# Kernel tuning notes

Measured on AMD Instinct MI355X. Metric: run time of the kernel, lower is better.

The kernel has to match this reference:

```python
import jax, jax.numpy as jnp
import numpy as np

B, T, D = 4, 2048, 1024
EPS = 1e-5


def _layernorm(x, g, b):
    mu = jnp.mean(x, axis=-1, keepdims=True)
    var = jnp.var(x, axis=-1, keepdims=True)
    return (x - mu) * jax.lax.rsqrt(var + EPS) * g + b


def setup_inputs() -> dict:
    key = jax.random.key(0)
    ks = jax.random.split(key, 16)
    s = lambda fan_in: 1.0 / np.sqrt(fan_in)
    return {
        "x": jax.random.normal(ks[0], (B, T, D), dtype=jnp.float32),
        "ln1_g": jnp.ones((D,), jnp.float32),
        "ln1_b": jnp.zeros((D,), jnp.float32),
        "Wqkv": jax.random.uniform(ks[1], (D, 3 * D), jnp.float32, -s(D), s(D)),
        "bqkv": jnp.zeros((3 * D,), jnp.float32),
        "Wproj": jax.random.uniform(ks[2], (D, D), jnp.float32, -s(D), s(D)),
        "bproj": jnp.zeros((D,), jnp.float32),
        "ln2_g": jnp.ones((D,), jnp.float32),
        "ln2_b": jnp.zeros((D,), jnp.float32),
        "W1": jax.random.uniform(ks[3], (D, 4 * D), jnp.float32, -s(D), s(D)),
        "b1": jnp.zeros((4 * D,), jnp.float32),
        "W2": jax.random.uniform(ks[4], (4 * D, D), jnp.float32, -s(4 * D), s(4 * D)),
        "b2": jnp.zeros((D,), jnp.float32),
    }


def reference(x, ln1_g, ln1_b, Wqkv, bqkv, Wproj, bproj, ln2_g, ln2_b, W1, b1, W2, b2):
    # NOTE: no residual connections in the original Block.
    h = _layernorm(x, ln1_g, ln1_b)
    kqv = h @ Wqkv + bqkv                      # [B,T,3D]
    k, q, v = jnp.split(kqv, 3, axis=-1)       # split order: k, q, v
    # Original scales by 1/sqrt(k.size(-1)) AFTER transposing k -> 1/sqrt(T).
    scores = jnp.einsum("btd,bsd->bts", q, k) * (1.0 / np.sqrt(T))
    causal = jnp.tril(jnp.ones((T, T), dtype=bool))
    scores = jnp.where(causal, scores, -jnp.inf)
    attn = jax.nn.softmax(scores, axis=-1)
    a = jnp.einsum("bts,bsd->btd", attn, v)
    a = a @ Wproj + bproj
    h2 = _layernorm(a, ln2_g, ln2_b)
    m = jax.nn.gelu(h2 @ W1 + b1, approximate=True)
    return m @ W2 + b2
```

## Files before the change

kernel.cpp:

```cpp
#include <hip/hip_runtime.h>
#include <hip/hip_bf16.h>

typedef __hip_bfloat16 bf16;
typedef __bf16 bf16x8 __attribute__((ext_vector_type(8)));
typedef __bf16 bf16x4 __attribute__((ext_vector_type(4)));
typedef float f32x4 __attribute__((ext_vector_type(4)));

static constexpr int Bq = 4, Tq = 2048, Dq = 1024;

__device__ inline float b2f(bf16 h) { return __bfloat162float(h); }
__device__ inline bf16 f2b(float f) { return __float2bfloat16(f); }

__device__ __forceinline__ void gload_lds16(const bf16* g, bf16* lds_wave_base) {
    __builtin_amdgcn_global_load_lds((const __attribute__((address_space(1))) void*)g,
                                     (__attribute__((address_space(3))) void*)lds_wave_base,
                                     16, 0, 0);
}

__device__ __forceinline__ float fast_gelu(float x) {
    float u = x * (0.7978845608028654f + 0.03567740814183427f * x * x);
    float e = __builtin_amdgcn_exp2f(-2.885390081777927f * u);
    return x * __builtin_amdgcn_rcpf(1.f + e);
}

__device__ inline void ld4f(const float* p, float* v) {
    float4 t = *reinterpret_cast<const float4*>(p);
    v[0] = t.x; v[1] = t.y; v[2] = t.z; v[3] = t.w;
}
__device__ inline void ld4f(const bf16* p, float* v) {
    bf16x4 t = *reinterpret_cast<const bf16x4*>(p);
    v[0] = (float)t[0]; v[1] = (float)t[1]; v[2] = (float)t[2]; v[3] = (float)t[3];
}

template <typename Tin>
__global__ void ln_kernel(const Tin* __restrict__ x, const float* __restrict__ g,
                          const float* __restrict__ b, bf16* __restrict__ out)
{
    const int row = blockIdx.x;
    const int tid = threadIdx.x;
    const int s0 = tid * 4;
    const Tin* xr = x + (size_t)row * Dq;
    bf16* orow = out + (size_t)row * Dq;
    float v[4], gv[4], bv[4];
    ld4f(xr + s0, v);
    ld4f(g + s0, gv);
    ld4f(b + s0, bv);
    float sum = v[0] + v[1] + v[2] + v[3];
    float sq = v[0]*v[0] + v[1]*v[1] + v[2]*v[2] + v[3]*v[3];
    for (int o = 32; o > 0; o >>= 1) { sum += __shfl_xor(sum, o); sq += __shfl_xor(sq, o); }
    __shared__ float ssum[4], ssq[4];
    const int w = tid >> 6;
    if ((tid & 63) == 0) { ssum[w] = sum; ssq[w] = sq; }
    __syncthreads();
    const float ts = ssum[0] + ssum[1] + ssum[2] + ssum[3];
    const float tq = ssq[0] + ssq[1] + ssq[2] + ssq[3];
    const float mean = ts / Dq;
    const float rs = rsqrtf(tq / Dq - mean * mean + 1e-5f);
    bf16x4 o4;
    #pragma unroll
    for (int i = 0; i < 4; ++i) o4[i] = (__bf16)((v[i] - mean) * rs * gv[i] + bv[i]);
    *reinterpret_cast<bf16x4*>(orow + s0) = o4;
}

__global__ void transpose_f2b_kernel(const float* __restrict__ in, bf16* __restrict__ out,
                                     long ldin, long ldout)
{
    __shared__ float tile[32][33];
    const int c0 = blockIdx.x * 32, r0 = blockIdx.y * 32;
    const int tx = threadIdx.x, ty = threadIdx.y;
    for (int i = 0; i < 4; ++i) {
        int r = r0 + ty + i * 8;
        tile[ty + i * 8][tx] = in[(size_t)r * ldin + c0 + tx];
    }
    __syncthreads();
    for (int i = 0; i < 4; ++i) {
        int cc = ty + i * 8;
        out[(size_t)(c0 + cc) * ldout + r0 + tx] = f2b(tile[tx][cc]);
    }
}

__global__ void transpose_b2b_kernel(const bf16* __restrict__ in, bf16* __restrict__ out,
                                     long ldin, long ldout, long inBatch, long outBatch)
{
    __shared__ bf16 tile[32][33];
    const bf16* ip = in + (size_t)blockIdx.z * inBatch;
    bf16* op = out + (size_t)blockIdx.z * outBatch;
    const int c0 = blockIdx.x * 32, r0 = blockIdx.y * 32;
    const int tx = threadIdx.x, ty = threadIdx.y;
    for (int i = 0; i < 4; ++i) {
        int r = r0 + ty + i * 8;
        tile[ty + i * 8][tx] = ip[(size_t)r * ldin + c0 + tx];
    }
    __syncthreads();
    for (int i = 0; i < 4; ++i) {
        int cc = ty + i * 8;
        op[(size_t)(c0 + cc) * ldout + r0 + tx] = tile[tx][cc];
    }
}

__global__ void softmax_kernel(bf16* __restrict__ attn)
{
    const int row = blockIdx.x;
    const int bb = row >> 11;
    const int t = row & (Tq - 1);
    bf16* base = attn + (size_t)bb * Tq * Tq + (size_t)t * Tq;
    const int tid = threadIdx.x;
    const int len = t + 1;
    const int s0 = tid * 8;
    bf16x8 v8 = *reinterpret_cast<const bf16x8*>(base + s0);
    float ev[8];
    #pragma unroll
    for (int i = 0; i < 8; ++i) ev[i] = (s0 + i < len) ? (float)v8[i] : -1e30f;
    float mx = ev[0];
    #pragma unroll
    for (int i = 1; i < 8; ++i) mx = fmaxf(mx, ev[i]);
    for (int o = 32; o > 0; o >>= 1) mx = fmaxf(mx, __shfl_xor(mx, o));
    __shared__ float sred[4];
    const int w = tid >> 6;
    if ((tid & 63) == 0) sred[w] = mx;
    __syncthreads();
    mx = fmaxf(fmaxf(sred[0], sred[1]), fmaxf(sred[2], sred[3]));
    __syncthreads();
    float sum = 0.f;
    #pragma unroll
    for (int i = 0; i < 8; ++i) {
        ev[i] = (s0 + i < len) ? __builtin_amdgcn_exp2f(1.4426950408889634f * (ev[i] - mx)) : 0.f;
        sum += ev[i];
    }
    for (int o = 32; o > 0; o >>= 1) sum += __shfl_xor(sum, o);
    if ((tid & 63) == 0) sred[w] = sum;
    __syncthreads();
    const float inv = __builtin_amdgcn_rcpf(sred[0] + sred[1] + sred[2] + sred[3]);
    bf16x8 o8;
    #pragma unroll
    for (int i = 0; i < 8; ++i) o8[i] = (__bf16)(ev[i] * inv);
    *reinterpret_cast<bf16x8*>(base + s0) = o8;
}

__global__ void gemm128(const bf16* __restrict__ A, const bf16* __restrict__ Bt,
                        const float* __restrict__ bias,
                        bf16* __restrict__ Cb, float* __restrict__ Cf,
                        int K, long lda, long ldb, long ldc,
                        long sA, long sB, long sC,
                        float scale, int act, int causal, int causalK)
{
    const int gx = gridDim.x, gy = gridDim.y;
    int lin = blockIdx.x + gx * blockIdx.y;
    const int band = lin & 7;
    const int idx = lin >> 3;
    const int bx = idx % gx;
    const int by = band * (gy >> 3) + idx / gx;

    const int m0 = by * 128, n0 = bx * 128;
    if (causal && n0 > m0 + 127) return;
    const int Kend = causalK ? min(K, m0 + 128) : K;

    __shared__ bf16 As[128 * 32];
    __shared__ bf16 Bs[128 * 32];

    const bf16* Ab = A + (size_t)blockIdx.z * sA;
    const bf16* Bb = Bt + (size_t)blockIdx.z * sB;
    const int tid = threadIdx.x;
    const int wid = tid >> 6, lane = tid & 63;
    const int wr = wid >> 1, wc = wid & 1;
    const int l15 = lane & 15, quad = lane >> 4;

    const int srow = wid * 16 + (lane >> 2);
    const int scol = (((lane & 3) ^ ((srow >> 1) & 3))) * 8;
    const bf16* agp0 = Ab + (size_t)(m0 + srow) * lda + scol;
    const bf16* agp1 = Ab + (size_t)(m0 + 64 + srow) * lda + scol;
    const bf16* bgp0 = Bb + (size_t)(n0 + srow) * ldb + scol;
    const bf16* bgp1 = Bb + (size_t)(n0 + 64 + srow) * ldb + scol;
    bf16* aw0 = As + wid * 512;
    bf16* aw1 = As + 2048 + wid * 512;
    bf16* bw0 = Bs + wid * 512;
    bf16* bw1 = Bs + 2048 + wid * 512;

    const int xsw = (l15 >> 1) & 3;
    const int afo = (wr * 64 + l15) * 32 + (quad ^ xsw) * 8;
    const int bfo = (wc * 64 + l15) * 32 + (quad ^ xsw) * 8;

    f32x4 acc[4][4];
    #pragma unroll
    for (int i = 0; i < 4; ++i)
        #pragma unroll
        for (int j = 0; j < 4; ++j) acc[i][j] = (f32x4){0.f, 0.f, 0.f, 0.f};

    for (int k0 = 0; k0 < Kend; k0 += 32) {
        gload_lds16(agp0 + k0, aw0);
        gload_lds16(agp1 + k0, aw1);
        gload_lds16(bgp0 + k0, bw0);
        gload_lds16(bgp1 + k0, bw1);
        __syncthreads();

        bf16x8 af[4], bff[4];
        #pragma unroll
        for (int i = 0; i < 4; ++i) af[i] = *reinterpret_cast<const bf16x8*>(As + afo + i * 512);
        #pragma unroll
        for (int j = 0; j < 4; ++j) bff[j] = *reinterpret_cast<const bf16x8*>(Bs + bfo + j * 512);
        #pragma unroll
        for (int i = 0; i < 4; ++i)
            #pragma unroll
            for (int j = 0; j < 4; ++j)
                acc[i][j] = __builtin_amdgcn_mfma_f32_16x16x32_bf16(af[i], bff[j], acc[i][j], 0, 0, 0);

        __syncthreads();
    }

    #pragma unroll
    for (int i = 0; i < 4; ++i) {
        const int row = m0 + wr * 64 + i * 16 + quad * 4;
        #pragma unroll
        for (int j = 0; j < 4; ++j) {
            const int col = n0 + wc * 64 + j * 16 + l15;
            const float bv = bias ? bias[col] : 0.f;
            #pragma unroll
            for (int r = 0; r < 4; ++r) {
                float vv = scale * acc[i][j][r] + bv;
                if (act == 1) vv = fast_gelu(vv);
                const size_t idx2 = (size_t)(row + r) * ldc + col + (size_t)blockIdx.z * sC;
                if (Cf) Cf[idx2] = vv;
                else    Cb[idx2] = f2b(vv);
            }
        }
    }
}

extern "C" void kernel_launch(void* const* d_in, const int* in_sizes, int n_in,
                              void* d_out, int out_size, void* d_ws, size_t ws_size,
                              hipStream_t stream)
{
    (void)in_sizes; (void)n_in; (void)out_size; (void)ws_size;
    const float* x     = (const float*)d_in[0];
    const float* ln1g  = (const float*)d_in[1];
    const float* ln1b  = (const float*)d_in[2];
    const float* Wqkv  = (const float*)d_in[3];
    const float* bqkv  = (const float*)d_in[4];
    const float* Wproj = (const float*)d_in[5];
    const float* bproj = (const float*)d_in[6];
    const float* ln2g  = (const float*)d_in[7];
    const float* ln2b  = (const float*)d_in[8];
    const float* W1    = (const float*)d_in[9];
    const float* b1    = (const float*)d_in[10];
    const float* W2    = (const float*)d_in[11];
    const float* b2    = (const float*)d_in[12];
    float* out = (float*)d_out;

    char* ws = (char*)d_ws;
    size_t off = 0;
    auto alloc = [&](size_t elems) { bf16* p = (bf16*)(ws + off); off += elems * sizeof(bf16); return p; };
    bf16* WqkvT  = alloc(3072UL * 1024);
    bf16* WprojT = alloc(1024UL * 1024);
    bf16* W1T    = alloc(4096UL * 1024);
    bf16* W2T    = alloc(1024UL * 4096);
    bf16* h      = alloc(8192UL * 1024);
    bf16* kqv    = alloc(8192UL * 3072);
    bf16* vT     = alloc(4UL * 1024 * 2048);
    bf16* attn   = alloc(4UL * 2048 * 2048);
    bf16* a   = h;
    bf16* p   = kqv;
    bf16* h2  = kqv + 8192UL * 1024;
    bf16* m   = kqv + 2UL * 8192 * 1024;

    const dim3 tb(32, 8);
    const long T3D = (long)Tq * 3072, TT = (long)Tq * Tq, DT = (long)Dq * Tq, TD = (long)Tq * Dq;

    transpose_f2b_kernel<<<dim3(96, 32), tb, 0, stream>>>(Wqkv,  WqkvT,  3072L, 1024L);
    transpose_f2b_kernel<<<dim3(32, 32), tb, 0, stream>>>(Wproj, WprojT, 1024L, 1024L);
    transpose_f2b_kernel<<<dim3(128, 32), tb, 0, stream>>>(W1,   W1T,    4096L, 1024L);
    transpose_f2b_kernel<<<dim3(32, 128), tb, 0, stream>>>(W2,   W2T,    1024L, 4096L);

    ln_kernel<float><<<8192, 256, 0, stream>>>(x, ln1g, ln1b, h);

    gemm128<<<dim3(24, 64, 1), 256, 0, stream>>>(h, WqkvT, bqkv, kqv, nullptr,
        1024, 1024L, 1024L, 3072L, 0L, 0L, 0L, 1.f, 0, 0, 0);

    transpose_b2b_kernel<<<dim3(32, 64, 4), tb, 0, stream>>>(kqv + 2048, vT, 3072L, 2048L, T3D, DT);

    gemm128<<<dim3(16, 16, 4), 256, 0, stream>>>(kqv + 1024, kqv, nullptr, attn, nullptr,
        1024, 3072L, 3072L, 2048L, T3D, T3D, TT, 0.022097086912079608f, 0, 1, 0);

    softmax_kernel<<<8192, 256, 0, stream>>>(attn);

    gemm128<<<dim3(8, 16, 4), 256, 0, stream>>>(attn, vT, nullptr, a, nullptr,
        2048, 2048L, 2048L, 1024L, TT, DT, TD, 1.f, 0, 0, 1);

    gemm128<<<dim3(8, 64, 1), 256, 0, stream>>>(a, WprojT, bproj, p, nullptr,
        1024, 1024L, 1024L, 1024L, 0L, 0L, 0L, 1.f, 0, 0, 0);

    ln_kernel<bf16><<<8192, 256, 0, stream>>>(p, ln2g, ln2b, h2);

    gemm128<<<dim3(32, 64, 1), 256, 0, stream>>>(h2, W1T, b1, m, nullptr,
        1024, 1024L, 1024L, 4096L, 0L, 0L, 0L, 1.f, 1, 0, 0);

    gemm128<<<dim3(8, 64, 1), 256, 0, stream>>>(m, W2T, b2, nullptr, out,
        4096, 4096L, 4096L, 1024L, 0L, 0L, 0L, 1.f, 0, 0, 0);
}
```

Before: 559.6 us.

## Fuse causal exp into QK GEMM, defer softmax normalization to PV GEMM

The QK^T GEMM epilogue now applies the causal mask and exp directly and writes unnormalized probabilities. A lightweight rowsum kernel computes each row's inverse sum, which the PV GEMM applies as a per-row output scale. This replaces the full read-modify-write softmax pass, and the QK GEMM launches only lower-triangular tiles through a triangular block index. The weight and V transposes are also retiled to 64x64 with paired bf16 stores. Dropping the max subtraction risks overflow if scores get large, and the row sums are taken from bf16-rounded values.

```diff
diff --git a/kernel.cpp b/kernel.cpp
--- a/kernel.cpp
+++ b/kernel.cpp
@@ -4,6 +4,7 @@
 typedef __hip_bfloat16 bf16;
 typedef __bf16 bf16x8 __attribute__((ext_vector_type(8)));
 typedef __bf16 bf16x4 __attribute__((ext_vector_type(4)));
+typedef __bf16 bf16x2 __attribute__((ext_vector_type(2)));
 typedef float f32x4 __attribute__((ext_vector_type(4)));
 
 static constexpr int Bq = 4, Tq = 2048, Dq = 1024;
@@ -65,94 +66,97 @@
 __global__ void transpose_f2b_kernel(const float* __restrict__ in, bf16* __restrict__ out,
                                      long ldin, long ldout)
 {
-    __shared__ float tile[32][33];
-    const int c0 = blockIdx.x * 32, r0 = blockIdx.y * 32;
-    const int tx = threadIdx.x, ty = threadIdx.y;
-    for (int i = 0; i < 4; ++i) {
-        int r = r0 + ty + i * 8;
-        tile[ty + i * 8][tx] = in[(size_t)r * ldin + c0 + tx];
+    __shared__ float tile[64][65];
+    const int c0 = blockIdx.x * 64, r0 = blockIdx.y * 64;
+    const int tid = threadIdx.x;
+    const int tx = tid & 63, ty = tid >> 6;
+    #pragma unroll
+    for (int i = 0; i < 16; ++i) {
+        int r = ty + i * 4;
+        tile[r][tx] = in[(size_t)(r0 + r) * ldin + c0 + tx];
     }
     __syncthreads();
-    for (int i = 0; i < 4; ++i) {
-        int cc = ty + i * 8;
-        out[(size_t)(c0 + cc) * ldout + r0 + tx] = f2b(tile[tx][cc]);
+    const int px = tid & 31, cy = tid >> 5;
+    #pragma unroll
+    for (int i = 0; i < 8; ++i) {
+        int cc = cy + i * 8;
+        bf16x2 p;
+        p[0] = (__bf16)tile[px * 2][cc];
+        p[1] = (__bf16)tile[px * 2 + 1][cc];
+        *reinterpret_cast<bf16x2*>(&out[(size_t)(c0 + cc) * ldout + r0 + px * 2]) = p;
     }
 }
 
 __global__ void transpose_b2b_kernel(const bf16* __restrict__ in, bf16* __restrict__ out,
                                      long ldin, long ldout, long inBatch, long outBatch)
 {
-    __shared__ bf16 tile[32][33];
+    __shared__ bf16 tile[64][66];
     const bf16* ip = in + (size_t)blockIdx.z * inBatch;
     bf16* op = out + (size_t)blockIdx.z * outBatch;
-    const int c0 = blockIdx.x * 32, r0 = blockIdx.y * 32;
-    const int tx = threadIdx.x, ty = threadIdx.y;
-    for (int i = 0; i < 4; ++i) {
-        int r = r0 + ty + i * 8;
-        tile[ty + i * 8][tx] = ip[(size_t)r * ldin + c0 + tx];
+    const int c0 = blockIdx.x * 64, r0 = blockIdx.y * 64;
+    const int tid = threadIdx.x;
+    const int tx = tid & 31, ty = tid >> 5;
+    #pragma unroll
+    for (int i = 0; i < 8; ++i) {
+        int r = ty + i * 8;
+        *reinterpret_cast<bf16x2*>(&tile[r][tx * 2]) =
+            *reinterpret_cast<const bf16x2*>(&ip[(size_t)(r0 + r) * ldin + c0 + tx * 2]);
     }
     __syncthreads();
-    for (int i = 0; i < 4; ++i) {
+    #pragma unroll
+    for (int i = 0; i < 8; ++i) {
         int cc = ty + i * 8;
-        op[(size_t)(c0 + cc) * ldout + r0 + tx] = tile[tx][cc];
-    }
-}
-
-__global__ void softmax_kernel(bf16* __restrict__ attn)
+        bf16x2 p;
+        p[0] = tile[tx * 2][cc];
+        p[1] = tile[tx * 2 + 1][cc];
+        *reinterpret_cast<bf16x2*>(&op[(size_t)(c0 + cc) * ldout + r0 + tx * 2]) = p;
+    }
+}
+
+__global__ void rowsum_kernel(const bf16* __restrict__ attn, float* __restrict__ invl)
 {
     const int row = blockIdx.x;
-    const int bb = row >> 11;
     const int t = row & (Tq - 1);
-    bf16* base = attn + (size_t)bb * Tq * Tq + (size_t)t * Tq;
+    const bf16* base = attn + (size_t)(row >> 11) * Tq * Tq + (size_t)t * Tq;
     const int tid = threadIdx.x;
     const int len = t + 1;
     const int s0 = tid * 8;
-    bf16x8 v8 = *reinterpret_cast<const bf16x8*>(base + s0);
-    float ev[8];
-    #pragma unroll
-    for (int i = 0; i < 8; ++i) ev[i] = (s0 + i < len) ? (float)v8[i] : -1e30f;
-    float mx = ev[0];
-    #pragma unroll
-    for (int i = 1; i < 8; ++i) mx = fmaxf(mx, ev[i]);
-    for (int o = 32; o > 0; o >>= 1) mx = fmaxf(mx, __shfl_xor(mx, o));
+    bf16x8 v = *reinterpret_cast<const bf16x8*>(base + s0);
+    float sum = 0.f;
+    #pragma unroll
+    for (int i = 0; i < 8; ++i) sum += (s0 + i < len) ? (float)v[i] : 0.f;
+    for (int o = 32; o > 0; o >>= 1) sum += __shfl_xor(sum, o);
     __shared__ float sred[4];
     const int w = tid >> 6;
-    if ((tid & 63) == 0) sred[w] = mx;
-    __syncthreads();
-    mx = fmaxf(fmaxf(sred[0], sred[1]), fmaxf(sred[2], sred[3]));
-    __syncthreads();
-    float sum = 0.f;
-    #pragma unroll
-    for (int i = 0; i < 8; ++i) {
-        ev[i] = (s0 + i < len) ? __builtin_amdgcn_exp2f(1.4426950408889634f * (ev[i] - mx)) : 0.f;
-        sum += ev[i];
-    }
-    for (int o = 32; o > 0; o >>= 1) sum += __shfl_xor(sum, o);
     if ((tid & 63) == 0) sred[w] = sum;
     __syncthreads();
-    const float inv = __builtin_amdgcn_rcpf(sred[0] + sred[1] + sred[2] + sred[3]);
-    bf16x8 o8;
-    #pragma unroll
-    for (int i = 0; i < 8; ++i) o8[i] = (__bf16)(ev[i] * inv);
-    *reinterpret_cast<bf16x8*>(base + s0) = o8;
+    if (tid == 0) invl[row] = 1.f / (sred[0] + sred[1] + sred[2] + sred[3]);
 }
 
 __global__ void gemm128(const bf16* __restrict__ A, const bf16* __restrict__ Bt,
-                        const float* __restrict__ bias,
+                        const float* __restrict__ bias, const float* __restrict__ rowscale,
                         bf16* __restrict__ Cb, float* __restrict__ Cf,
                         int K, long lda, long ldb, long ldc,
                         long sA, long sB, long sC,
-                        float scale, int act, int causal, int causalK)
-{
-    const int gx = gridDim.x, gy = gridDim.y;
-    int lin = blockIdx.x + gx * blockIdx.y;
-    const int band = lin & 7;
-    const int idx = lin >> 3;
-    const int bx = idx % gx;
-    const int by = band * (gy >> 3) + idx / gx;
+                        float scale, int act, int tri, int causalK)
+{
+    int bx, by;
+    if (tri) {
+        const int lin = blockIdx.x;
+        int t = (int)((sqrtf(8.f * lin + 1.f) - 1.f) * 0.5f);
+        while ((t + 1) * (t + 2) / 2 <= lin) ++t;
+        while (t * (t + 1) / 2 > lin) --t;
+        by = t; bx = lin - t * (t + 1) / 2;
+    } else {
+        const int gx = gridDim.x, gy = gridDim.y;
+        const int lin = blockIdx.x + gx * blockIdx.y;
+        const int band = lin & 7;
+        const int idx = lin >> 3;
+        bx = idx % gx;
+        by = band * (gy >> 3) + idx / gx;
+    }
 
     const int m0 = by * 128, n0 = bx * 128;
-    if (causal && n0 > m0 + 127) return;
     const int Kend = causalK ? min(K, m0 + 128) : K;
 
     __shared__ bf16 As[128 * 32];
@@ -207,6 +211,8 @@
         __syncthreads();
     }
 
+    const float* rsb = rowscale ? rowscale + (size_t)blockIdx.z * Tq : nullptr;
+
     #pragma unroll
     for (int i = 0; i < 4; ++i) {
         const int row = m0 + wr * 64 + i * 16 + quad * 4;
@@ -218,6 +224,9 @@
             for (int r = 0; r < 4; ++r) {
                 float vv = scale * acc[i][j][r] + bv;
                 if (act == 1) vv = fast_gelu(vv);
+                else if (act == 2)
+                    vv = (col <= row + r) ? __builtin_amdgcn_exp2f(1.4426950408889634f * vv) : 0.f;
+                if (rsb) vv *= rsb[row + r];
                 const size_t idx2 = (size_t)(row + r) * ldc + col + (size_t)blockIdx.z * sC;
                 if (Cf) Cf[idx2] = vv;
                 else    Cb[idx2] = f2b(vv);
@@ -257,42 +266,42 @@
     bf16* kqv    = alloc(8192UL * 3072);
     bf16* vT     = alloc(4UL * 1024 * 2048);
     bf16* attn   = alloc(4UL * 2048 * 2048);
+    float* invl  = (float*)alloc(8192UL * 2);
     bf16* a   = h;
     bf16* p   = kqv;
     bf16* h2  = kqv + 8192UL * 1024;
     bf16* m   = kqv + 2UL * 8192 * 1024;
 
-    const dim3 tb(32, 8);
     const long T3D = (long)Tq * 3072, TT = (long)Tq * Tq, DT = (long)Dq * Tq, TD = (long)Tq * Dq;
 
-    transpose_f2b_kernel<<<dim3(96, 32), tb, 0, stream>>>(Wqkv,  WqkvT,  3072L, 1024L);
-    transpose_f2b_kernel<<<dim3(32, 32), tb, 0, stream>>>(Wproj, WprojT, 1024L, 1024L);
-    transpose_f2b_kernel<<<dim3(128, 32), tb, 0, stream>>>(W1,   W1T,    4096L, 1024L);
-    transpose_f2b_kernel<<<dim3(32, 128), tb, 0, stream>>>(W2,   W2T,    1024L, 4096L);
+    transpose_f2b_kernel<<<dim3(48, 16), 256, 0, stream>>>(Wqkv,  WqkvT,  3072L, 1024L);
+    transpose_f2b_kernel<<<dim3(16, 16), 256, 0, stream>>>(Wproj, WprojT, 1024L, 1024L);
+    transpose_f2b_kernel<<<dim3(64, 16), 256, 0, stream>>>(W1,   W1T,    4096L, 1024L);
+    transpose_f2b_kernel<<<dim3(16, 64), 256, 0, stream>>>(W2,   W2T,    1024L, 4096L);
 
     ln_kernel<float><<<8192, 256, 0, stream>>>(x, ln1g, ln1b, h);
 
-    gemm128<<<dim3(24, 64, 1), 256, 0, stream>>>(h, WqkvT, bqkv, kqv, nullptr,
+    gemm128<<<dim3(24, 64, 1), 256, 0, stream>>>(h, WqkvT, bqkv, nullptr, kqv, nullptr,
         1024, 1024L, 1024L, 3072L, 0L, 0L, 0L, 1.f, 0, 0, 0);
 
-    transpose_b2b_kernel<<<dim3(32, 64, 4), tb, 0, stream>>>(kqv + 2048, vT, 3072L, 2048L, T3D, DT);
-
-    gemm128<<<dim3(16, 16, 4), 256, 0, stream>>>(kqv + 1024, kqv, nullptr, attn, nullptr,
-        1024, 3072L, 3072L, 2048L, T3D, T3D, TT, 0.022097086912079608f, 0, 1, 0);
-
-    softmax_kernel<<<8192, 256, 0, stream>>>(attn);
-
-    gemm128<<<dim3(8, 16, 4), 256, 0, stream>>>(attn, vT, nullptr, a, nullptr,
+    transpose_b2b_kernel<<<dim3(16, 32, 4), 256, 0, stream>>>(kqv + 2048, vT, 3072L, 2048L, T3D, DT);
+
+    gemm128<<<dim3(136, 1, 4), 256, 0, stream>>>(kqv + 1024, kqv, nullptr, nullptr, attn, nullptr,
+        1024, 3072L, 3072L, 2048L, T3D, T3D, TT, 0.022097086912079608f, 2, 1, 0);
+
+    rowsum_kernel<<<8192, 256, 0, stream>>>(attn, invl);
+
+    gemm128<<<dim3(8, 16, 4), 256, 0, stream>>>(attn, vT, nullptr, invl, a, nullptr,
         2048, 2048L, 2048L, 1024L, TT, DT, TD, 1.f, 0, 0, 1);
 
-    gemm128<<<dim3(8, 64, 1), 256, 0, stream>>>(a, WprojT, bproj, p, nullptr,
+    gemm128<<<dim3(8, 64, 1), 256, 0, stream>>>(a, WprojT, bproj, nullptr, p, nullptr,
         1024, 1024L, 1024L, 1024L, 0L, 0L, 0L, 1.f, 0, 0, 0);
 
     ln_kernel<bf16><<<8192, 256, 0, stream>>>(p, ln2g, ln2b, h2);
 
-    gemm128<<<dim3(32, 64, 1), 256, 0, stream>>>(h2, W1T, b1, m, nullptr,
+    gemm128<<<dim3(32, 64, 1), 256, 0, stream>>>(h2, W1T, b1, nullptr, m, nullptr,
         1024, 1024L, 1024L, 4096L, 0L, 0L, 0L, 1.f, 1, 0, 0);
 
-    gemm128<<<dim3(8, 64, 1), 256, 0, stream>>>(m, W2T, b2, nullptr, out,
+    gemm128<<<dim3(8, 64, 1), 256, 0, stream>>>(m, W2T, b2, nullptr, nullptr, out,
         4096, 4096L, 4096L, 1024L, 0L, 0L, 0L, 1.f, 0, 0, 0);
 }
```

Measured after the change: 552.7 us. No clear change (-1.2%).
